# Kernel tuning notes

Hardware: AMD Instinct MI355X
Metric: run time of the kernel (lower is better)

The kernel has to match this reference:

```python
import jax, jax.numpy as jnp
import numpy as np
import math

B, S, MEM, D, H = 2, 2048, 512, 1024, 16
DH = D // H  # 64


def setup_inputs() -> dict:
    key = jax.random.key(0)
    ks = jax.random.split(key, 12)
    s = 1.0 / math.sqrt(D)
    return {
        "x": jax.random.normal(ks[0], (B, S, D), jnp.float32),
        "mems": jax.random.normal(ks[1], (B, MEM, D), jnp.float32),
        "freqs_cis": jax.random.normal(ks[2], (S, 32), jnp.float32),
        "mask": jax.random.randint(ks[3], (B, MEM + S), 0, 2, jnp.int32),
        "Wq": jax.random.normal(ks[4], (D, D), jnp.float32) * s,
        "bq": jnp.zeros((D,), jnp.float32),
        "Wk": jax.random.normal(ks[5], (D, D), jnp.float32) * s,
        "bk": jnp.zeros((D,), jnp.float32),
        "Wv": jax.random.normal(ks[6], (D, D), jnp.float32) * s,
        "bv": jnp.zeros((D,), jnp.float32),
        "Wo": jax.random.normal(ks[7], (D, D), jnp.float32) * s,
        "bo": jnp.zeros((D,), jnp.float32),
    }


def _split_heads(t):
    # [B, T, D] -> [B, H, T, DH]
    b, t_, _ = t.shape
    return t.reshape(b, t_, H, DH).transpose(0, 2, 1, 3)


def reference(x, mems, freqs_cis, mask, Wq, bq, Wk, bk, Wv, bv, Wo, bo):
    # mems prepended along sequence for K/V (torch: c = cat([mems, x], 1))
    c = jnp.concatenate([mems, x], axis=1)  # [B, MEM+S, D]
    Q = _split_heads(x @ Wq.T + bq)          # [B, H, S, DH]
    K = _split_heads(c @ Wk.T + bk)          # [B, H, Skv, DH]
    V = _split_heads(c @ Wv.T + bv)          # [B, H, Skv, DH]

    scores = jnp.einsum("bhqd,bhkd->bhqk", Q, K) / math.sqrt(DH)
    m = mask.astype(jnp.float32)             # [B, Skv]
    scores = scores - 1e6 * (1.0 - m[:, None, None, :])
    attn = jax.nn.softmax(scores, axis=-1)   # dropout omitted (eval mode)
    out = jnp.einsum("bhqk,bhkd->bhqd", attn, V)  # [B, H, S, DH]
    out = out.transpose(0, 2, 1, 3).reshape(B, S, D)
    return out @ Wo.T + bo
```

## Files before the change

kernel.cpp:

```cpp
#include <hip/hip_runtime.h>
#include <math.h>

#define NB   2
#define SQ   2048
#define SMEM 512
#define SKVN 2560
#define ND   1024
#define NH   16
#define DHN  64
#define NBH  32

typedef unsigned short u16;
typedef short bf16x8 __attribute__((ext_vector_type(8)));
typedef float f32x4 __attribute__((ext_vector_type(4)));
typedef u16 u16x4 __attribute__((ext_vector_type(4)));
typedef u16 u16x8 __attribute__((ext_vector_type(8)));

#define CSC   0.1803368801111204f

__device__ __forceinline__ u16 f2bf(float f) {
    unsigned u = __float_as_uint(f);
    u += 0x7FFFu + ((u >> 16) & 1u);
    return (u16)(u >> 16);
}

__device__ __forceinline__ void async16(u16* lds, const u16* g) {
    __builtin_amdgcn_global_load_lds(
        (const __attribute__((address_space(1))) void*)g,
        (__attribute__((address_space(3))) void*)lds, 16, 0, 0);
}

__device__ __forceinline__ unsigned lds_off(const void* p) {
    return (unsigned)(uintptr_t)(const __attribute__((address_space(3))) void*)p;
}

__device__ __forceinline__ u16x4 tr_read(unsigned a) {
    u16x4 d;
    asm volatile("ds_read_b64_tr_b16 %0, %1" : "=v"(d) : "v"(a) : "memory");
    return d;
}

__device__ __forceinline__ unsigned cvtpk(float lo, float hi) {
    unsigned r;
    asm("v_cvt_pk_bf16_f32 %0, %1, %2" : "=v"(r) : "v"(lo), "v"(hi));
    return r;
}

__device__ __forceinline__ float exp2r(float x) {
    float r;
    asm("v_exp_f32 %0, %1" : "=v"(r) : "v"(x));
    return r;
}

union PKU { unsigned u[2]; u16x4 v; };
union U8  { struct { u16x4 lo, hi; } p; bf16x8 v; };

__global__ __launch_bounds__(256)
void cvt_all(const float* __restrict__ x, const float* __restrict__ mems,
             const float* __restrict__ W0, const float* __restrict__ W1,
             const float* __restrict__ W2, const float* __restrict__ W3,
             u16* __restrict__ xb, u16* __restrict__ memb,
             u16* __restrict__ d0, u16* __restrict__ d1,
             u16* __restrict__ d2, u16* __restrict__ d3,
             const int* __restrict__ mask, float* __restrict__ mbias)
{
    const int bid = blockIdx.x;
    if (bid >= 4608) {
        const int i = (bid - 4608) * 256 + threadIdx.x;
        if (i < NB * SKVN) mbias[i] = mask[i] ? 0.f : 1.0e6f * CSC;
        return;
    }
    size_t i = ((size_t)bid * 256 + threadIdx.x) * 8;
    const float* s; u16* d;
    if (i < 4194304) { s = x; d = xb; }
    else if (i < 5242880) { s = mems; d = memb; i -= 4194304; }
    else {
        size_t off = i - 5242880;
        const int wi = (int)(off >> 20);
        i = off & 1048575;
        switch (wi) {
            case 0:  s = W0; d = d0; break;
            case 1:  s = W1; d = d1; break;
            case 2:  s = W2; d = d2; break;
            default: s = W3; d = d3; break;
        }
    }
    float4 a = *(const float4*)(s + i);
    float4 b = *(const float4*)(s + i + 4);
    u16x8 o;
    o[0]=f2bf(a.x); o[1]=f2bf(a.y); o[2]=f2bf(a.z); o[3]=f2bf(a.w);
    o[4]=f2bf(b.x); o[5]=f2bf(b.y); o[6]=f2bf(b.z); o[7]=f2bf(b.w);
    *(u16x8*)(d + i) = o;
}

__device__ __forceinline__ const u16* arow_ptr(const u16* x, const u16* mems,
                                               int grow, int T, int memLen) {
    int b = grow >= T ? 1 : 0;
    int t = grow - b * T;
    if (memLen > 0 && t < memLen)
        return mems + ((size_t)(b * memLen + t)) * ND;
    return x + ((size_t)(b * (T - memLen) + (t - memLen))) * ND;
}

__device__ __forceinline__
void gemm_body(const u16* __restrict__ x, const u16* __restrict__ mems,
               const u16* __restrict__ W, const float* __restrict__ bias,
               void* __restrict__ out, int T, int memLen, int mode,
               int bx, int by, u16* As0, u16* As1, u16* Bs0, u16* Bs1)
{
    u16* As[2] = {As0, As1};
    u16* Bs[2] = {Bs0, Bs1};

    const int tid  = threadIdx.x;
    const int wave = tid >> 6, lane = tid & 63;
    const int lg = lane >> 4, li = lane & 15;
    const int wr = (wave >> 1) * 64, wc = (wave & 1) * 64;
    const int row0 = bx * 128, col0 = by * 128;

    const int srow = lane >> 2;
    const int sslot = lane & 3;

    f32x4 acc[4][4];
    const f32x4 zf = {0.f, 0.f, 0.f, 0.f};
#pragma unroll
    for (int m = 0; m < 4; ++m)
#pragma unroll
        for (int n = 0; n < 4; ++n) acc[m][n] = zf;

    auto stage = [&](int c, int kt) {
        const int k0 = kt * 32;
#pragma unroll
        for (int ch = wave; ch < 8; ch += 4) {
            const int r = ch * 16 + srow;
            const int gs = sslot ^ ((r ^ (r >> 2)) & 3);
            async16(&As[c][ch * 512],
                    arow_ptr(x, mems, row0 + r, T, memLen) + k0 + gs * 8);
        }
#pragma unroll
        for (int ch = wave; ch < 8; ch += 4) {
            const int r = ch * 16 + srow;
            const int gs = sslot ^ ((r ^ (r >> 2)) & 3);
            async16(&Bs[c][ch * 512],
                    W + (size_t)(col0 + r) * ND + k0 + gs * 8);
        }
    };

    stage(0, 0);
    int cur = 0;
    for (int kt = 0; kt < 32; ++kt) {
        __syncthreads();
        if (kt + 1 < 32) stage(cur ^ 1, kt + 1);

        bf16x8 af[4], bfr[4];
#pragma unroll
        for (int m = 0; m < 4; ++m) {
            const int r = wr + m * 16 + li;
            af[m] = *(const bf16x8*)&As[cur][r * 32 + ((lg ^ ((r ^ (r >> 2)) & 3)) << 3)];
        }
#pragma unroll
        for (int n = 0; n < 4; ++n) {
            const int r = wc + n * 16 + li;
            bfr[n] = *(const bf16x8*)&Bs[cur][r * 32 + ((lg ^ ((r ^ (r >> 2)) & 3)) << 3)];
        }
#pragma unroll
        for (int m = 0; m < 4; ++m)
#pragma unroll
            for (int n = 0; n < 4; ++n)
                acc[m][n] = __builtin_amdgcn_mfma_f32_16x16x32_bf16(
                                af[m], bfr[n], acc[m][n], 0, 0, 0);
        cur ^= 1;
    }

#pragma unroll
    for (int n = 0; n < 4; ++n) {
        const int col = col0 + wc + n * 16 + li;
        const float bv = bias[col];
#pragma unroll
        for (int m = 0; m < 4; ++m) {
            const int rbase = row0 + wr + m * 16 + 4 * lg;
            if (mode == 1) {
                u16* o = (u16*)out;
                const int h = col >> 6, dh = col & 63;
#pragma unroll
                for (int r = 0; r < 4; ++r) {
                    const int grow = rbase + r;
                    const int b = grow >= T ? 1 : 0;
                    const int t = grow - b * T;
                    o[(((size_t)b * NH + h) * T + t) * DHN + dh] =
                        f2bf(acc[m][n][r] + bv);
                }
            } else {
                u16* o = (u16*)out;
                const int h = col >> 6, dh = col & 63;
                const int b = rbase >= T ? 1 : 0;
                const int t = rbase - b * T;
                u16x4 pk;
                pk[0] = f2bf(acc[m][n][0] + bv);
                pk[1] = f2bf(acc[m][n][1] + bv);
                pk[2] = f2bf(acc[m][n][2] + bv);
                pk[3] = f2bf(acc[m][n][3] + bv);
                *(u16x4*)&o[(((size_t)b * NH + h) * DHN + dh) * (size_t)T + t] = pk;
            }
        }
    }
}

__global__ __launch_bounds__(256)
void gemm_qkv(const u16* __restrict__ xb, const u16* __restrict__ memb,
              const u16* __restrict__ Wq, const float* __restrict__ bq, u16* Qb,
              const u16* __restrict__ Wk, const float* __restrict__ bk, u16* Kb,
              const u16* __restrict__ Wv, const float* __restrict__ bv, u16* Vtb)
{
    __shared__ u16 As[2][128 * 32];
    __shared__ u16 Bs[2][128 * 32];
    const int id = (blockIdx.x & 7) * 112 + (blockIdx.x >> 3);
    if (id < 256) {
        gemm_body(xb, nullptr, Wq, bq, Qb, SQ, 0, 1, id & 31, id >> 5,
                  As[0], As[1], Bs[0], Bs[1]);
    } else if (id < 576) {
        const int t = id - 256;
        gemm_body(xb, memb, Wk, bk, Kb, SKVN, SMEM, 1, t % 40, t / 40,
                  As[0], As[1], Bs[0], Bs[1]);
    } else {
        const int t = id - 576;
        gemm_body(xb, memb, Wv, bv, Vtb, SKVN, SMEM, 2, t % 40, t / 40,
                  As[0], As[1], Bs[0], Bs[1]);
    }
}

__global__ __launch_bounds__(256)
void gemm_o(const u16* __restrict__ x, const u16* __restrict__ W,
            const float* __restrict__ bias, float* __restrict__ out)
{
    __shared__ u16 As[2][64 * 32];
    __shared__ u16 Bs[2][128 * 32];

    const int tid  = threadIdx.x;
    const int wave = tid >> 6, lane = tid & 63;
    const int lg = lane >> 4, li = lane & 15;
    const int wr = (wave >> 1) * 32, wc = (wave & 1) * 64;

    const int id = (blockIdx.x & 7) * 64 + (blockIdx.x >> 3);
    const int row0 = (id >> 3) * 64, col0 = (id & 7) * 128;

    const int srow = lane >> 2;
    const int sslot = lane & 3;

    f32x4 acc[2][4];
    const f32x4 zf = {0.f, 0.f, 0.f, 0.f};
#pragma unroll
    for (int m = 0; m < 2; ++m)
#pragma unroll
        for (int n = 0; n < 4; ++n) acc[m][n] = zf;

    auto stage = [&](int c, int kt) {
        const int k0 = kt * 32;
        {
            const int r = wave * 16 + srow;
            const int gs = sslot ^ ((r ^ (r >> 2)) & 3);
            async16(&As[c][wave * 512],
                    x + (size_t)(row0 + r) * ND + k0 + gs * 8);
        }
#pragma unroll
        for (int ch = wave; ch < 8; ch += 4) {
            const int r = ch * 16 + srow;
            const int gs = sslot ^ ((r ^ (r >> 2)) & 3);
            async16(&Bs[c][ch * 512],
                    W + (size_t)(col0 + r) * ND + k0 + gs * 8);
        }
    };

    stage(0, 0);
    int cur = 0;
    for (int kt = 0; kt < 32; ++kt) {
        __syncthreads();
        if (kt + 1 < 32) stage(cur ^ 1, kt + 1);

        bf16x8 af[2], bfr[4];
#pragma unroll
        for (int m = 0; m < 2; ++m) {
            const int r = wr + m * 16 + li;
            af[m] = *(const bf16x8*)&As[cur][r * 32 + ((lg ^ ((r ^ (r >> 2)) & 3)) << 3)];
        }
#pragma unroll
        for (int n = 0; n < 4; ++n) {
            const int r = wc + n * 16 + li;
            bfr[n] = *(const bf16x8*)&Bs[cur][r * 32 + ((lg ^ ((r ^ (r >> 2)) & 3)) << 3)];
        }
#pragma unroll
        for (int m = 0; m < 2; ++m)
#pragma unroll
            for (int n = 0; n < 4; ++n)
                acc[m][n] = __builtin_amdgcn_mfma_f32_16x16x32_bf16(
                                af[m], bfr[n], acc[m][n], 0, 0, 0);
        cur ^= 1;
    }

#pragma unroll
    for (int n = 0; n < 4; ++n) {
        const int col = col0 + wc + n * 16 + li;
        const float bv = bias[col];
#pragma unroll
        for (int m = 0; m < 2; ++m) {
            const int rbase = row0 + wr + m * 16 + 4 * lg;
#pragma unroll
            for (int r = 0; r < 4; ++r)
                out[(size_t)(rbase + r) * ND + col] = acc[m][n][r] + bv;
        }
    }
}

__global__ __launch_bounds__(256)
void attn_mfma(const u16* __restrict__ Qw, const u16* __restrict__ Kw,
               const u16* __restrict__ Vt, const float* __restrict__ mbias,
               u16* __restrict__ AO)
{
    __shared__ u16 Ks[2][64 * 64];
    __shared__ u16 Vs[2][64 * 64];
    __shared__ u16 Ps[4][2048];

    const int tid  = threadIdx.x;
    const int wave = tid >> 6, lane = tid & 63;
    const int lg = lane >> 4, li = lane & 15;

    const int wg = blockIdx.x;
    const int sw = (wg & 7) * 64 + (wg >> 3);
    const int bh = sw >> 4;
    const int q0 = (sw & 15) * 128;
    const int b = bh >> 4, h = bh & 15;

    const u16* Kg = Kw + (size_t)bh * SKVN * DHN;
    const u16* Vg = Vt + (size_t)bh * DHN * SKVN;
    const float* mrow = mbias + (size_t)b * SKVN;

    bf16x8 qA0, qA1, qB0, qB1;
    {
        const u16* Qp = Qw + ((size_t)bh * SQ + q0 + wave * 32 + li) * DHN;
        qA0 = *(const bf16x8*)(Qp + lg * 8);
        qA1 = *(const bf16x8*)(Qp + 32 + lg * 8);
        qB0 = *(const bf16x8*)(Qp + 16 * DHN + lg * 8);
        qB1 = *(const bf16x8*)(Qp + 16 * DHN + 32 + lg * 8);
    }

    U8 ou;
#pragma unroll
    for (int i = 0; i < 4; ++i) { ou.p.lo[i] = 0x3F80; ou.p.hi[i] = 0x3F80; }
    const bf16x8 onesb = ou.v;

    const int srow = lane >> 3, sslot = lane & 7;

    auto stage = [&](int c, int t) {
        const int kv0 = t * 64;
#pragma unroll
        for (int ch = wave; ch < 8; ch += 4) {
            const int r = ch * 8 + srow;
            async16(&Ks[c][ch * 512],
                    Kg + (size_t)(kv0 + r) * DHN + ((sslot ^ (r & 7)) << 3));
        }
#pragma unroll
        for (int ch = wave; ch < 8; ch += 4) {
            const int r = ch * 8 + srow;
            async16(&Vs[c][ch * 512],
                    Vg + (size_t)r * SKVN + kv0 + ((sslot ^ (r & 7)) << 3));
        }
    };

    f32x4 oA[4], oB[4], laccA, laccB;
    const f32x4 zf = {0.f, 0.f, 0.f, 0.f};
#pragma unroll
    for (int n = 0; n < 4; ++n) { oA[n] = zf; oB[n] = zf; }
    laccA = zf; laccB = zf;

    u16* Pw = &Ps[wave][0];
    const unsigned paA = lds_off(Pw) + 256u * lg + 8u * li;
    const unsigned paB = paA + 2048u;

    float mbn[4];
#pragma unroll
    for (int n = 0; n < 4; ++n) mbn[n] = mrow[n * 16 + li];

    stage(0, 0);
    int cur = 0;
    for (int t = 0; t < SKVN / 64; ++t) {
        float mbc[4];
#pragma unroll
        for (int n = 0; n < 4; ++n) mbc[n] = mbn[n];

        __syncthreads();
        if (t + 1 < SKVN / 64) {
            stage(cur ^ 1, t + 1);
#pragma unroll
            for (int n = 0; n < 4; ++n)
                mbn[n] = mrow[(t + 1) * 64 + n * 16 + li];
        }

        __builtin_amdgcn_s_setprio(1);
        f32x4 sA[4], sB[4];
#pragma unroll
        for (int n = 0; n < 4; ++n) {
            const int r = n * 16 + li;
            bf16x8 kb0 = *(const bf16x8*)&Ks[cur][r * 64 + ((lg ^ (r & 7)) << 3)];
            bf16x8 kb1 = *(const bf16x8*)&Ks[cur][r * 64 + (((4 + lg) ^ (r & 7)) << 3)];
            f32x4 z = zf;
            z     = __builtin_amdgcn_mfma_f32_16x16x32_bf16(qA0, kb0, z, 0, 0, 0);
            sA[n] = __builtin_amdgcn_mfma_f32_16x16x32_bf16(qA1, kb1, z, 0, 0, 0);
            f32x4 y = zf;
            y     = __builtin_amdgcn_mfma_f32_16x16x32_bf16(qB0, kb0, y, 0, 0, 0);
            sB[n] = __builtin_amdgcn_mfma_f32_16x16x32_bf16(qB1, kb1, y, 0, 0, 0);
        }
        __builtin_amdgcn_s_setprio(0);

#pragma unroll
        for (int n = 0; n < 4; ++n) {
            const float mb = mbc[n];
            const int pw = (n * 16 + li) * 16 + lg * 4;
            PKU ua;
            ua.u[0] = cvtpk(exp2r(fmaf(sA[n][0], CSC, -mb)),
                            exp2r(fmaf(sA[n][1], CSC, -mb)));
            ua.u[1] = cvtpk(exp2r(fmaf(sA[n][2], CSC, -mb)),
                            exp2r(fmaf(sA[n][3], CSC, -mb)));
            *(u16x4*)&Pw[pw] = ua.v;
            PKU ub;
            ub.u[0] = cvtpk(exp2r(fmaf(sB[n][0], CSC, -mb)),
                            exp2r(fmaf(sB[n][1], CSC, -mb)));
            ub.u[1] = cvtpk(exp2r(fmaf(sB[n][2], CSC, -mb)),
                            exp2r(fmaf(sB[n][3], CSC, -mb)));
            *(u16x4*)&Pw[1024 + pw] = ub.v;
        }

        u16x4 a00 = tr_read(paA);
        u16x4 a01 = tr_read(paA + 128);
        u16x4 a10 = tr_read(paA + 1024);
        u16x4 a11 = tr_read(paA + 1024 + 128);
        u16x4 b00 = tr_read(paB);
        u16x4 b01 = tr_read(paB + 128);
        u16x4 b10 = tr_read(paB + 1024);
        u16x4 b11 = tr_read(paB + 1024 + 128);
        asm volatile("s_waitcnt lgkmcnt(0)" ::: "memory");
        __builtin_amdgcn_sched_barrier(0);
        U8 pA0, pA1, pB0, pB1;
        pA0.p.lo = a00; pA0.p.hi = a01;
        pA1.p.lo = a10; pA1.p.hi = a11;
        pB0.p.lo = b00; pB0.p.hi = b01;
        pB1.p.lo = b10; pB1.p.hi = b11;

        __builtin_amdgcn_s_setprio(1);
        laccA = __builtin_amdgcn_mfma_f32_16x16x32_bf16(pA0.v, onesb, laccA, 0, 0, 0);
        laccA = __builtin_amdgcn_mfma_f32_16x16x32_bf16(pA1.v, onesb, laccA, 0, 0, 0);
        laccB = __builtin_amdgcn_mfma_f32_16x16x32_bf16(pB0.v, onesb, laccB, 0, 0, 0);
        laccB = __builtin_amdgcn_mfma_f32_16x16x32_bf16(pB1.v, onesb, laccB, 0, 0, 0);
#pragma unroll
        for (int n = 0; n < 4; ++n) {
            const int r = n * 16 + li;
            bf16x8 vb0 = *(const bf16x8*)&Vs[cur][r * 64 + ((lg ^ (r & 7)) << 3)];
            bf16x8 vb1 = *(const bf16x8*)&Vs[cur][r * 64 + (((4 + lg) ^ (r & 7)) << 3)];
            oA[n] = __builtin_amdgcn_mfma_f32_16x16x32_bf16(pA0.v, vb0, oA[n], 0, 0, 0);
            oA[n] = __builtin_amdgcn_mfma_f32_16x16x32_bf16(pA1.v, vb1, oA[n], 0, 0, 0);
            oB[n] = __builtin_amdgcn_mfma_f32_16x16x32_bf16(pB0.v, vb0, oB[n], 0, 0, 0);
            oB[n] = __builtin_amdgcn_mfma_f32_16x16x32_bf16(pB1.v, vb1, oB[n], 0, 0, 0);
        }
        __builtin_amdgcn_s_setprio(0);
        cur ^= 1;
    }

#pragma unroll
    for (int r = 0; r < 4; ++r) {
        const float invA = 1.f / laccA[r];
        const float invB = 1.f / laccB[r];
        const int rowA = q0 + wave * 32 + 4 * lg + r;
#pragma unroll
        for (int n = 0; n < 4; ++n) {
            const int col = h * DHN + n * 16 + li;
            AO[((size_t)b * SQ + rowA) * ND + col] = f2bf(oA[n][r] * invA);
            AO[((size_t)b * SQ + rowA + 16) * ND + col] = f2bf(oB[n][r] * invB);
        }
    }
}

extern "C" void kernel_launch(void* const* d_in, const int* in_sizes, int n_in,
                              void* d_out, int out_size, void* d_ws, size_t ws_size,
                              hipStream_t stream)
{
    const float* x    = (const float*)d_in[0];
    const float* mems = (const float*)d_in[1];
    const int*   mask = (const int*)d_in[3];
    const float* Wq = (const float*)d_in[4];  const float* bq = (const float*)d_in[5];
    const float* Wk = (const float*)d_in[6];  const float* bk = (const float*)d_in[7];
    const float* Wv = (const float*)d_in[8];  const float* bv = (const float*)d_in[9];
    const float* Wo = (const float*)d_in[10]; const float* bo = (const float*)d_in[11];
    float* out = (float*)d_out;

    u16* ws = (u16*)d_ws;
    u16* xb   = ws;
    u16* memb = xb   + (size_t)NB * SQ * ND;
    u16* Wqb  = memb + (size_t)NB * SMEM * ND;
    u16* Wkb  = Wqb + (size_t)ND * ND;
    u16* Wvb  = Wkb + (size_t)ND * ND;
    u16* Wob  = Wvb + (size_t)ND * ND;
    u16* Qb   = Wob + (size_t)ND * ND;
    u16* Kb   = Qb  + (size_t)NB * NH * SQ * DHN;
    u16* Vtb  = Kb  + (size_t)NB * NH * SKVN * DHN;
    u16* AOb  = Vtb + (size_t)NB * NH * SKVN * DHN;
    float* mbias = (float*)(AOb + (size_t)NB * SQ * ND);

    const dim3 blk(256);
    cvt_all<<<dim3(4628), blk, 0, stream>>>(x, mems, Wq, Wk, Wv, Wo,
                                            xb, memb, Wqb, Wkb, Wvb, Wob,
                                            mask, mbias);
    gemm_qkv<<<dim3(896), blk, 0, stream>>>(xb, memb,
                                            Wqb, bq, Qb,
                                            Wkb, bk, Kb,
                                            Wvb, bv, Vtb);
    attn_mfma<<<dim3(512), blk, 0, stream>>>(Qb, Kb, Vtb, mbias, AOb);
    gemm_o<<<dim3(512), blk, 0, stream>>>(AOb, Wob, bo, out);
}
```

Measured before the change: 165.7 us.

## Prefetch attention K/V two tiles ahead with explicit waitcnts and LDS-resident mask

The attention kernel now issues K/V loads for tiles t and t+1 up front and refills a buffer with tile t+2 after each iteration, using explicit vmcnt/lgkmcnt waits and raw barriers in place of __syncthreads. The mask bias is stored as bf16 and the whole row is copied into LDS once per block, so per-tile global mask loads go away. The aim is to keep more memory traffic in flight and hide load latency behind the MFMA work. The cost is an extra barrier per iteration and a hand-counted vmcnt that assumes a fixed number of outstanding loads per stage.

After: 164.0 us. Within noise of the previous version (-1.0%).

```diff
diff --git a/kernel.cpp b/kernel.cpp
--- a/kernel.cpp
+++ b/kernel.cpp
@@ -24,6 +24,10 @@
     return (u16)(u >> 16);
 }
 
+__device__ __forceinline__ float bf2f(u16 v) {
+    return __uint_as_float(((unsigned)v) << 16);
+}
+
 __device__ __forceinline__ void async16(u16* lds, const u16* g) {
     __builtin_amdgcn_global_load_lds(
         (const __attribute__((address_space(1))) void*)g,
@@ -62,12 +66,13 @@
              u16* __restrict__ xb, u16* __restrict__ memb,
              u16* __restrict__ d0, u16* __restrict__ d1,
              u16* __restrict__ d2, u16* __restrict__ d3,
-             const int* __restrict__ mask, float* __restrict__ mbias)
+             const int* __restrict__ mask, u16* __restrict__ mb16)
 {
     const int bid = blockIdx.x;
     if (bid >= 4608) {
         const int i = (bid - 4608) * 256 + threadIdx.x;
-        if (i < NB * SKVN) mbias[i] = mask[i] ? 0.f : 1.0e6f * CSC;
+        if (i < NB * SKVN)
+            mb16[i] = mask[i] ? (u16)0 : f2bf(1.0e6f * CSC);
         return;
     }
     size_t i = ((size_t)bid * 256 + threadIdx.x) * 8;
@@ -312,12 +317,13 @@
 
 __global__ __launch_bounds__(256)
 void attn_mfma(const u16* __restrict__ Qw, const u16* __restrict__ Kw,
-               const u16* __restrict__ Vt, const float* __restrict__ mbias,
+               const u16* __restrict__ Vt, const u16* __restrict__ mb16,
                u16* __restrict__ AO)
 {
     __shared__ u16 Ks[2][64 * 64];
     __shared__ u16 Vs[2][64 * 64];
     __shared__ u16 Ps[4][2048];
+    __shared__ u16 Ms[SKVN];
 
     const int tid  = threadIdx.x;
     const int wave = tid >> 6, lane = tid & 63;
@@ -331,7 +337,7 @@
 
     const u16* Kg = Kw + (size_t)bh * SKVN * DHN;
     const u16* Vg = Vt + (size_t)bh * DHN * SKVN;
-    const float* mrow = mbias + (size_t)b * SKVN;
+    const u16* m16row = mb16 + (size_t)b * SKVN;
 
     bf16x8 qA0, qA1, qB0, qB1;
     {
@@ -342,6 +348,9 @@
         qB1 = *(const bf16x8*)(Qp + 16 * DHN + 32 + lg * 8);
     }
 
+    for (int i = tid * 8; i < SKVN; i += 2048)
+        *(u16x8*)&Ms[i] = *(const u16x8*)(m16row + i);
+
     U8 ou;
 #pragma unroll
     for (int i = 0; i < 4; ++i) { ou.p.lo[i] = 0x3F80; ou.p.hi[i] = 0x3F80; }
@@ -375,24 +384,25 @@
     const unsigned paA = lds_off(Pw) + 256u * lg + 8u * li;
     const unsigned paB = paA + 2048u;
 
-    float mbn[4];
-#pragma unroll
-    for (int n = 0; n < 4; ++n) mbn[n] = mrow[n * 16 + li];
-
+    __syncthreads();
+    __builtin_amdgcn_sched_barrier(0);
     stage(0, 0);
+    __builtin_amdgcn_sched_barrier(0);
+    stage(1, 1);
+    __builtin_amdgcn_sched_barrier(0);
+
+    const int NT = SKVN / 64;
     int cur = 0;
-    for (int t = 0; t < SKVN / 64; ++t) {
+    for (int t = 0; t < NT; ++t) {
+        if (t == NT - 1) asm volatile("s_waitcnt vmcnt(0)" ::: "memory");
+        else             asm volatile("s_waitcnt vmcnt(4)" ::: "memory");
+        __builtin_amdgcn_s_barrier();
+        __builtin_amdgcn_sched_barrier(0);
+
         float mbc[4];
 #pragma unroll
-        for (int n = 0; n < 4; ++n) mbc[n] = mbn[n];
-
-        __syncthreads();
-        if (t + 1 < SKVN / 64) {
-            stage(cur ^ 1, t + 1);
-#pragma unroll
-            for (int n = 0; n < 4; ++n)
-                mbn[n] = mrow[(t + 1) * 64 + n * 16 + li];
-        }
+        for (int n = 0; n < 4; ++n)
+            mbc[n] = bf2f(Ms[t * 64 + n * 16 + li]);
 
         __builtin_amdgcn_s_setprio(1);
         f32x4 sA[4], sB[4];
@@ -460,6 +470,12 @@
             oB[n] = __builtin_amdgcn_mfma_f32_16x16x32_bf16(pB1.v, vb1, oB[n], 0, 0, 0);
         }
         __builtin_amdgcn_s_setprio(0);
+
+        asm volatile("s_waitcnt lgkmcnt(0)" ::: "memory");
+        __builtin_amdgcn_s_barrier();
+        __builtin_amdgcn_sched_barrier(0);
+
+        if (t + 2 < NT) stage(cur, t + 2);
         cur ^= 1;
     }
 
@@ -501,16 +517,16 @@
     u16* Kb   = Qb  + (size_t)NB * NH * SQ * DHN;
     u16* Vtb  = Kb  + (size_t)NB * NH * SKVN * DHN;
     u16* AOb  = Vtb + (size_t)NB * NH * SKVN * DHN;
-    float* mbias = (float*)(AOb + (size_t)NB * SQ * ND);
+    u16* mb16 = AOb + (size_t)NB * SQ * ND;
 
     const dim3 blk(256);
     cvt_all<<<dim3(4628), blk, 0, stream>>>(x, mems, Wq, Wk, Wv, Wo,
                                             xb, memb, Wqb, Wkb, Wvb, Wob,
-                                            mask, mbias);
+                                            mask, mb16);
     gemm_qkv<<<dim3(896), blk, 0, stream>>>(xb, memb,
                                             Wqb, bq, Qb,
                                             Wkb, bk, Kb,
                                             Wvb, bv, Vtb);
-    attn_mfma<<<dim3(512), blk, 0, stream>>>(Qb, Kb, Vtb, mbias, AOb);
+    attn_mfma<<<dim3(512), blk, 0, stream>>>(Qb, Kb, Vtb, mb16, AOb);
     gemm_o<<<dim3(512), blk, 0, stream>>>(AOb, Wob, bo, out);
 }
```
